# Optimization experiments

Hardware: AMD Instinct MI355X
Metric: run time of the kernel (lower is better)

## Reference

```python
import jax, jax.numpy as jnp
import numpy as np

IN_F, OUT_F, NB = 4096, 4096, 8
BS = IN_F // NB  # 512


def setup_inputs() -> dict:
    key = jax.random.key(0)
    k1, k2, k3, k4 = jax.random.split(key, 4)
    weight = jax.random.normal(k1, (OUT_F, IN_F), dtype=jnp.float32) * 0.02
    bias = jax.random.normal(k2, (OUT_F,), dtype=jnp.float32) * 0.02
    x = jax.random.normal(k3, (4, 2048, IN_F), dtype=jnp.float32)
    R_blocks = jax.random.normal(k4, (NB, BS, BS), dtype=jnp.float32) * 0.1
    return {"weight": weight, "bias": bias, "x": x, "R_blocks": R_blocks, "layer_idx": 0}


def cayley_transform(A):
    # A: [nb, bs, bs]; Q = (I - A_skew) @ inv(I + A_skew + 1e-6 I)
    bs = A.shape[-1]
    I = jnp.eye(bs, dtype=A.dtype)
    A_skew = 0.5 * (A - jnp.swapaxes(A, -2, -1))
    return jnp.matmul(I - A_skew, jnp.linalg.inv(I + A_skew + 1e-6 * I))


def reference(weight, bias, x, R_blocks, layer_idx):
    R_ortho = cayley_transform(R_blocks)  # [nb, bs, bs]
    # weight @ block_diag(R) == per-block contraction on the in_features axis
    w = weight.reshape(OUT_F, NB, BS)
    tw = jnp.einsum('onb,nbc->onc', w, R_ortho).reshape(OUT_F, IN_F)
    # F.linear: x @ tw.T + bias
    out = jnp.einsum('bsi,oi->bso', x, tw) + bias
    return out
```

## Files before the change

### kernel.cpp

```cpp
#include <hip/hip_runtime.h>
#include <hip/hip_bf16.h>


typedef unsigned short u16;
typedef __attribute__((ext_vector_type(8))) __bf16 bf16x8;
typedef __attribute__((ext_vector_type(4))) float f32x4;
typedef __attribute__((ext_vector_type(8))) unsigned short u16x8;
typedef __attribute__((ext_vector_type(4))) unsigned short u16x4;

#define C0   1.000001f
#define C1Q  2.000001f
#define AS1 __attribute__((address_space(1)))
#define AS3 __attribute__((address_space(3)))

__device__ __forceinline__ u16 f2bf(float x) {
  union { float f; unsigned u; } v; v.f = x;
  return (u16)((v.u + 0x7fffu + ((v.u >> 16) & 1u)) >> 16);
}
__device__ __forceinline__ float bf2f(u16 h) {
  union { float f; unsigned u; } v; v.u = ((unsigned)h) << 16; return v.f;
}

__global__ __launch_bounds__(256) void k_build_M(const float* __restrict__ R,
                                                 u16* __restrict__ Mh,
                                                 u16* __restrict__ Ml) {
  __shared__ float t1[32][33];
  const int n = blockIdx.z;
  const int tr = blockIdx.y * 32, tc = blockIdx.x * 32;
  const int ly = threadIdx.x >> 5, lx = threadIdx.x & 31;
  const float* Rb = R + (size_t)n * 262144;
  float a[4];
#pragma unroll
  for (int i = 0; i < 4; ++i) {
    a[i] = Rb[(size_t)(tr + ly + i * 8) * 512 + tc + lx];
    t1[ly + i * 8][lx] = Rb[(size_t)(tc + ly + i * 8) * 512 + tr + lx];
  }
  __syncthreads();
#pragma unroll
  for (int i = 0; i < 4; ++i) {
    const int r = tr + ly + i * 8, c = tc + lx;
    float m = 0.5f * (a[i] - t1[lx][ly + i * 8]) + (r == c ? C0 : 0.0f);
    u16 h = f2bf(m);
    const size_t idx = (size_t)n * 262144 + (size_t)r * 512 + c;
    Mh[idx] = h;
    Ml[idx] = f2bf(m - bf2f(h));
  }
}

__global__ __launch_bounds__(1024) void k_frob_alpha(const u16* __restrict__ G4,
                                                     float* __restrict__ alpha) {
  __shared__ float red[16];
  const int n = blockIdx.x, tid = threadIdx.x;
  const u16* src = G4 + (size_t)n * 262144;
  float s = 0.f;
  for (int i = tid; i < 32768; i += 1024) {
    u16x8 v = reinterpret_cast<const u16x8*>(src)[i];
#pragma unroll
    for (int e = 0; e < 8; ++e) { float f = bf2f(v[e]); s += f * f; }
  }
  for (int off = 32; off; off >>= 1) s += __shfl_down(s, off, 64);
  if ((tid & 63) == 0) red[tid >> 6] = s;
  __syncthreads();
  if (tid == 0) {
    float t = 0.f;
    for (int q = 0; q < 16; ++q) t += red[q];
    float lam = powf(t, 0.125f);
    alpha[n] = 2.0f / (C0 * C0 + lam);
  }
}

__global__ __launch_bounds__(256) void k_init_X0(const u16* __restrict__ Mh,
                                                 const u16* __restrict__ Ml,
                                                 const float* __restrict__ alpha,
                                                 u16* __restrict__ X0,
                                                 u16* __restrict__ X0t) {
  int idx = blockIdx.x * 256 + threadIdx.x;
  int n = idx >> 18, r = (idx >> 9) & 511, c = idx & 511;
  float m = bf2f(Mh[idx]) + bf2f(Ml[idx]);
  float a = alpha[n];
  X0[idx]  = f2bf(a * ((r == c ? 2.0f * C0 : 0.0f) - m));
  X0t[idx] = f2bf(a * m);
}

template <int PROD3, int DMODE, int OMODE>
__global__ __launch_bounds__(256)
void k_bmm(const u16* __restrict__ Ah, const u16* __restrict__ Al,
           const u16* __restrict__ Bh, const u16* __restrict__ Bl,
           const u16* __restrict__ Dh, const u16* __restrict__ Dl,
           u16* __restrict__ Cnh, u16* __restrict__ Cnl,
           u16* __restrict__ Cth, u16* __restrict__ Ctl,
           float* __restrict__ Cf, float cd, float cs) {
  __shared__ __align__(16) u16 sAh[2048], sBh[2048];
  __shared__ __align__(16) u16 sAl[PROD3 ? 2048 : 8], sBl[PROD3 ? 2048 : 8];
  const size_t zb = (size_t)blockIdx.z * 262144;
  const int tid = threadIdx.x, lane = tid & 63, wave = tid >> 6;
  const int m0 = blockIdx.y * 64, n0 = blockIdx.x * 64;
  const int wr = wave >> 1, wc = wave & 1;
  const int c15 = lane & 15, lk = lane >> 4;
  const int srow = tid >> 2;
  const int sg = (tid & 3) ^ (srow & 3);
  f32x4 acc[2][2] = {};
  const u16* pa = Ah + zb + (size_t)(m0 + srow) * 512 + sg * 8;
  const u16* pb = Bh + zb + (size_t)(n0 + srow) * 512 + sg * 8;

  for (int k0 = 0; k0 < 512; k0 += 32) {
    __builtin_amdgcn_global_load_lds((const AS1 void*)(pa + k0),
                                     (AS3 void*)(sAh + (size_t)tid * 8), 16, 0, 0);
    __builtin_amdgcn_global_load_lds((const AS1 void*)(pb + k0),
                                     (AS3 void*)(sBh + (size_t)tid * 8), 16, 0, 0);
    if constexpr (PROD3) {
      const u16* pal = Al + zb + (size_t)(m0 + srow) * 512 + sg * 8;
      const u16* pbl = Bl + zb + (size_t)(n0 + srow) * 512 + sg * 8;
      __builtin_amdgcn_global_load_lds((const AS1 void*)(pal + k0),
                                       (AS3 void*)(sAl + (size_t)tid * 8), 16, 0, 0);
      __builtin_amdgcn_global_load_lds((const AS1 void*)(pbl + k0),
                                       (AS3 void*)(sBl + (size_t)tid * 8), 16, 0, 0);
    }
    __syncthreads();
    bf16x8 a[2], b[2], al2[2], bl2[2];
#pragma unroll
    for (int i = 0; i < 2; ++i) {
      const int fr = wr * 32 + i * 16 + c15;
      const int ia = fr * 32 + ((lk ^ (fr & 3)) * 8);
      a[i] = *reinterpret_cast<const bf16x8*>(&sAh[ia]);
      if constexpr (PROD3) al2[i] = *reinterpret_cast<const bf16x8*>(&sAl[ia]);
    }
#pragma unroll
    for (int j = 0; j < 2; ++j) {
      const int fc = wc * 32 + j * 16 + c15;
      const int ib = fc * 32 + ((lk ^ (fc & 3)) * 8);
      b[j] = *reinterpret_cast<const bf16x8*>(&sBh[ib]);
      if constexpr (PROD3) bl2[j] = *reinterpret_cast<const bf16x8*>(&sBl[ib]);
    }
#pragma unroll
    for (int i = 0; i < 2; ++i)
#pragma unroll
      for (int j = 0; j < 2; ++j) {
        acc[i][j] = __builtin_amdgcn_mfma_f32_16x16x32_bf16(a[i], b[j], acc[i][j], 0, 0, 0);
        if constexpr (PROD3) {
          acc[i][j] = __builtin_amdgcn_mfma_f32_16x16x32_bf16(a[i],   bl2[j], acc[i][j], 0, 0, 0);
          acc[i][j] = __builtin_amdgcn_mfma_f32_16x16x32_bf16(al2[i], b[j],   acc[i][j], 0, 0, 0);
        }
      }
    __syncthreads();
  }
#pragma unroll
  for (int i = 0; i < 2; ++i)
#pragma unroll
    for (int j = 0; j < 2; ++j) {
      const int rowb = m0 + wr * 32 + i * 16 + lk * 4;
      const int col  = n0 + wc * 32 + j * 16 + c15;
      u16 hv[4], lv[4];
#pragma unroll
      for (int r = 0; r < 4; ++r) {
        float val = cs * acc[i][j][r];
        if constexpr (DMODE >= 1) {
          float d = bf2f(Dh[zb + (size_t)(rowb + r) * 512 + col]);
          if constexpr (DMODE == 2) d += bf2f(Dl[zb + (size_t)(rowb + r) * 512 + col]);
          val += cd * d;
        }
        if constexpr (OMODE & 16) Cf[zb + (size_t)(rowb + r) * 512 + col] = val;
        u16 h = f2bf(val);
        if constexpr (OMODE & 1) Cnh[zb + (size_t)(rowb + r) * 512 + col] = h;
        u16 l = 0;
        if constexpr (OMODE & 10) l = f2bf(val - bf2f(h));
        if constexpr (OMODE & 2) Cnl[zb + (size_t)(rowb + r) * 512 + col] = l;
        hv[r] = h; lv[r] = l;
      }
      if constexpr (OMODE & 4) {
        u16x4 v; v[0] = hv[0]; v[1] = hv[1]; v[2] = hv[2]; v[3] = hv[3];
        *reinterpret_cast<u16x4*>(&Cth[zb + (size_t)col * 512 + rowb]) = v;
      }
      if constexpr (OMODE & 8) {
        u16x4 v; v[0] = lv[0]; v[1] = lv[1]; v[2] = lv[2]; v[3] = lv[3];
        *reinterpret_cast<u16x4*>(&Ctl[zb + (size_t)col * 512 + rowb]) = v;
      }
    }
}

template <int SPLIT, int BF16OUT>
__global__ __launch_bounds__(256)
void k_smm(const float* __restrict__ A, int lda, long long astride,
           const float* __restrict__ B, int ldb, long long bstride,
           void* __restrict__ Cv, int ldc, long long cstride,
           const float* __restrict__ D, int ldd, long long dstride,
           float c1, float sgn, int K) {
  __shared__ __align__(16) u16 lA  [128 * 40];
  __shared__ __align__(16) u16 lBT [128 * 40];
  const int nz = blockIdx.z;
  const float* Ab = A + (size_t)nz * astride;
  const float* Bb = B + (size_t)nz * bstride;
  const float* Db = D + (size_t)nz * dstride;
  const int tid = threadIdx.x, lane = tid & 63, wave = tid >> 6;
  const int m0 = blockIdx.y * 128, n0 = blockIdx.x * 128;
  const int wr = wave >> 1, wc = wave & 1;
  f32x4 acc[4][4] = {};

  for (int k0 = 0; k0 < K; k0 += 32) {
    if (k0) __syncthreads();
    {
      const int row = tid >> 1, ks = (tid & 1) * 16;
      const float* src = Ab + (size_t)(m0 + row) * lda + k0 + ks;
      float fv[16];
#pragma unroll
      for (int q = 0; q < 4; ++q) {
        float4 f = *(reinterpret_cast<const float4*>(src) + q);
        fv[q * 4 + 0] = f.x; fv[q * 4 + 1] = f.y; fv[q * 4 + 2] = f.z; fv[q * 4 + 3] = f.w;
      }
      u16x8 w0, w1;
#pragma unroll
      for (int e = 0; e < 8; ++e) { w0[e] = f2bf(fv[e]); w1[e] = f2bf(fv[e + 8]); }
      *reinterpret_cast<u16x8*>(&lA[row * 40 + ks])     = w0;
      *reinterpret_cast<u16x8*>(&lA[row * 40 + ks + 8]) = w1;
    }
    {
      const int kk = tid >> 3, nb = (tid & 7) * 16;
      const float* src = Bb + (size_t)(k0 + kk) * ldb + n0 + nb;
      float fv[16];
#pragma unroll
      for (int q = 0; q < 4; ++q) {
        float4 f = *(reinterpret_cast<const float4*>(src) + q);
        fv[q * 4 + 0] = f.x; fv[q * 4 + 1] = f.y; fv[q * 4 + 2] = f.z; fv[q * 4 + 3] = f.w;
      }
#pragma unroll
      for (int e = 0; e < 16; ++e) lBT[(nb + e) * 40 + kk] = f2bf(fv[e]);
    }
    __syncthreads();
    const int ks = (lane >> 4) * 8;
    bf16x8 af[4], bfr[4];
#pragma unroll
    for (int f = 0; f < 4; ++f) {
      const int ar = wr * 64 + f * 16 + (lane & 15);
      const int bc = wc * 64 + f * 16 + (lane & 15);
      af[f]  = *reinterpret_cast<const bf16x8*>(&lA [ar * 40 + ks]);
      bfr[f] = *reinterpret_cast<const bf16x8*>(&lBT[bc * 40 + ks]);
    }
#pragma unroll
    for (int i = 0; i < 4; ++i)
#pragma unroll
      for (int j = 0; j < 4; ++j)
        acc[i][j] = __builtin_amdgcn_mfma_f32_16x16x32_bf16(af[i], bfr[j], acc[i][j], 0, 0, 0);
  }
#pragma unroll
  for (int i = 0; i < 4; ++i) {
    const int rowb = m0 + wr * 64 + i * 16 + ((lane >> 4) << 2);
#pragma unroll
    for (int j = 0; j < 4; ++j) {
      const int col = n0 + wc * 64 + j * 16 + (lane & 15);
#pragma unroll
      for (int r = 0; r < 4; ++r) {
        float val = sgn * acc[i][j][r];
        if (c1 != 0.0f) val += c1 * Db[(size_t)(rowb + r) * ldd + col];
        if constexpr (BF16OUT)
          reinterpret_cast<u16*>(Cv)[(size_t)nz * cstride + (size_t)(rowb + r) * ldc + col] = f2bf(val);
        else
          reinterpret_cast<float*>(Cv)[(size_t)nz * cstride + (size_t)(rowb + r) * ldc + col] = val;
      }
    }
  }
}

__global__ __launch_bounds__(256) void k_f32_to_bf16(const float* __restrict__ in,
                                                     u16* __restrict__ out) {
  int idx = blockIdx.x * 256 + threadIdx.x;
  const float* src = in + (size_t)idx * 8;
  float4 f0 = *reinterpret_cast<const float4*>(src);
  float4 f1 = *reinterpret_cast<const float4*>(src + 4);
  u16x8 w;
  w[0] = f2bf(f0.x); w[1] = f2bf(f0.y); w[2] = f2bf(f0.z); w[3] = f2bf(f0.w);
  w[4] = f2bf(f1.x); w[5] = f2bf(f1.y); w[6] = f2bf(f1.z); w[7] = f2bf(f1.w);
  *reinterpret_cast<u16x8*>(out + (size_t)idx * 8) = w;
}

#define NSLOT 9

#define RD_B(dst, G)                                                           \
  _Pragma("unroll")                                                            \
  for (int n = 0; n < 4; ++n)                                                  \
    dst[n] = *reinterpret_cast<const bf16x8*>(                                 \
        &lds[bslot * 8192 + (bro + n * 16) * 64 + (G) * 8]);

#define RD_A(dst, MH, G)                                                       \
  _Pragma("unroll")                                                            \
  for (int m = 0; m < 4; ++m)                                                  \
    dst[m] = *reinterpret_cast<const bf16x8*>(                                 \
        &lds[aslot * 8192 + ((MH) * 64 + m * 16 + c15) * 64 + (G) * 8]);

#define MFMA16(afX, bfX, MH)                                                   \
  __builtin_amdgcn_s_setprio(1);                                               \
  _Pragma("unroll")                                                            \
  for (int m = 0; m < 4; ++m)                                                  \
    _Pragma("unroll")                                                          \
    for (int n = 0; n < 4; ++n)                                                \
      acc[(MH) * 4 + m][n] = __builtin_amdgcn_mfma_f32_16x16x32_bf16(          \
          afX[m], bfX[n], acc[(MH) * 4 + m][n], 0, 0, 0);                      \
  __builtin_amdgcn_s_setprio(0);                                               \
  __builtin_amdgcn_sched_barrier(0);

#define SBAR() __builtin_amdgcn_s_barrier();
#define SCHB() __builtin_amdgcn_sched_barrier(0);

#define TILEBODY(WM, LAST)                                                     \
  {                              \
    STAGE();                                                                   \
    RD_A(afB, 1, gsA)                                                          \
    SCHB()                                                                     \
    MFMA16(afA, bf0, 0)                                                        \
    SBAR()                                                                     \
                             \
    STAGE();                                                                   \
    RD_B(bf1, gsB)                                                             \
    RD_A(afA, 0, gsB)                                                          \
    SCHB()                                                                     \
    MFMA16(afB, bf0, 1)                                                        \
    SBAR()                                                                     \
                                 \
    STAGE();                                                                   \
    RD_A(afB, 1, gsB)                                                          \
    SCHB()                                                                     \
    MFMA16(afA, bf1, 0)                                                        \
    SBAR()                                                                     \
        \
    STAGE();                                                                   \
    if ((WM) == 1) { asm volatile("s_waitcnt vmcnt(2)" ::: "memory"); SCHB() } \
    if ((WM) == 2) { asm volatile("s_waitcnt vmcnt(0)" ::: "memory"); SCHB() } \
    SBAR()                                                                     \
    ADV()                                                                      \
    if (!(LAST)) { RD_B(bf0, gsA) RD_A(afA, 0, gsA) }                          \
    SCHB()                                                                     \
    MFMA16(afB, bf1, 1)                                                        \
    SBAR()                                                                     \
  }

#define ADV()                                                                  \
  aslot += 4; if (aslot >= NSLOT) aslot -= NSLOT;                              \
  bslot += 4; if (bslot >= NSLOT) bslot -= NSLOT;

__global__ __launch_bounds__(512, 2)
void k_gemm256(const u16* __restrict__ A, const u16* __restrict__ B,
               const float* __restrict__ bias,
               float* __restrict__ C, int N, int K) {
  __shared__ __align__(16) u16 lds[NSLOT * 8192];
  const int tid = threadIdx.x, lane = tid & 63, wave = tid >> 6;
  int bid = blockIdx.y * gridDim.x + blockIdx.x;
  const int cpx = (gridDim.x * gridDim.y) >> 3;
  bid = (bid & 7) * cpx + (bid >> 3);
  const int nbx = N >> 8;
  const int bx = bid % nbx, by = bid / nbx;
  const int m0 = by << 8, n0 = bx << 8;
  const int wr = wave >> 2, wc = wave & 3;
  const int srow = tid >> 3;
  const int scg  = (tid & 7) ^ (srow & 7);
  const int c15 = lane & 15, lq = lane >> 4;
  const int gs0 = lq ^ (lane & 7);
  const int gsA = gs0, gsB = gs0 ^ 4;
  const int bro = (wc & 1) * 64 + c15;
  const int NT = K >> 6;

  f32x4 acc[8][4] = {};
  bf16x8 afA[4], afB[4], bf0[4], bf1[4];

  int jn = 0, jslot = 0;
  auto STAGE = [&]() {
    if (jn < 4 * NT) {
      const int tau_s = jn >> 2, qh = jn & 3;
      const u16* srcb = (qh < 2)
          ? A + (size_t)(m0 + (qh & 1) * 128 + srow) * (size_t)K
          : B + (size_t)(n0 + (qh & 1) * 128 + srow) * (size_t)K;
      const u16* src = srcb + (tau_s << 6) + scg * 8;
      u16* dst = (u16*)lds + jslot * 8192 + wave * 512;
      __builtin_amdgcn_global_load_lds(
          (const AS1 void*)src, (AS3 void*)dst, 16, 0, 0);
      __builtin_amdgcn_global_load_lds(
          (const AS1 void*)(src + (size_t)64 * K), (AS3 void*)(dst + 4096), 16, 0, 0);
    }
    ++jn; jslot = (jslot == NSLOT - 1) ? 0 : jslot + 1;
  };

  STAGE(); STAGE(); STAGE(); STAGE(); STAGE(); STAGE();
  asm volatile("s_waitcnt vmcnt(4)" ::: "memory");
  SCHB()
  SBAR()
  int aslot = wr, bslot = 2 + (wc >> 1);
  RD_B(bf0, gsA)
  RD_A(afA, 0, gsA)
  SCHB()

  for (int tau = 0; tau < NT - 2; ++tau) {
    TILEBODY(1, 0)
  }
  TILEBODY(2, 0)
  TILEBODY(0, 1)

#pragma unroll
  for (int n = 0; n < 4; ++n) {
    const int col = n0 + wc * 64 + n * 16 + c15;
    const float bv = bias[col];
#pragma unroll
    for (int mi = 0; mi < 8; ++mi) {
      const int rowb = m0 + wr * 128 + mi * 16 + (lq << 2);
#pragma unroll
      for (int r = 0; r < 4; ++r)
        C[(size_t)(rowb + r) * N + col] = acc[mi][n][r] + bv;
    }
  }
}

extern "C" void kernel_launch(void* const* d_in, const int* in_sizes, int n_in,
                              void* d_out, int out_size, void* d_ws, size_t ws_size,
                              hipStream_t stream) {
  const float* W    = (const float*)d_in[0];
  const float* bias = (const float*)d_in[1];
  const float* x    = (const float*)d_in[2];
  const float* R    = (const float*)d_in[3];
  float* out = (float*)d_out;

  char* ws = (char*)d_ws;
  u16* x_bf = (u16*)(ws);
  u16* tw   = (u16*)(ws + 67108864);

  char* arena = (char*)d_out;
  auto slot = [&](int i) -> u16* { return (u16*)(arena + (size_t)i * 4194304); };
  u16 *Mh = slot(0), *Ml = slot(1);
  u16 *G = slot(2), *G2 = slot(3), *G4 = slot(4);
  u16 *Xa = slot(5), *Xat = slot(6), *Xb = slot(7), *Xbt = slot(8);
  u16 *Xbl = slot(9), *Xbtl = slot(10);
  u16 *Tt = slot(2);
  u16 *Tth = slot(3), *Ttl = slot(4);
  u16 *X6h = slot(5), *X6l = slot(6);
  u16 *X6th = slot(11), *X6tl = slot(12);
  float* Qf = (float*)(arena + (size_t)13 * 4194304);
  float* alpha = (float*)(arena + (size_t)15 * 4194304);

  const long long BS2 = 262144;
  const dim3 g8(8, 8, 8);
  const u16* NUL = nullptr;

  k_build_M<<<dim3(16, 16, 8), 256, 0, stream>>>(R, Mh, Ml);
  k_bmm<0, 0, 1><<<g8, 256, 0, stream>>>(Mh, NUL, Mh, NUL, NUL, NUL,
                                         G, nullptr, nullptr, nullptr, nullptr, 0.f, 1.f);
  k_bmm<0, 0, 1><<<g8, 256, 0, stream>>>(G, NUL, G, NUL, NUL, NUL,
                                         G2, nullptr, nullptr, nullptr, nullptr, 0.f, 1.f);
  k_bmm<0, 0, 1><<<g8, 256, 0, stream>>>(G2, NUL, G2, NUL, NUL, NUL,
                                         G4, nullptr, nullptr, nullptr, nullptr, 0.f, 1.f);
  k_frob_alpha<<<8, 1024, 0, stream>>>(G4, alpha);
  k_init_X0<<<8192, 256, 0, stream>>>(Mh, Ml, alpha, Xa, Xat);

  u16 *cur = Xa, *curt = Xat, *nxt = Xb, *nxtt = Xbt;
  for (int it = 0; it < 4; ++it) {
    k_bmm<0, 0, 4><<<g8, 256, 0, stream>>>(Mh, NUL, curt, NUL, NUL, NUL,
                                           nullptr, nullptr, Tt, nullptr, nullptr, 0.f, 1.f);
    k_bmm<0, 1, 5><<<g8, 256, 0, stream>>>(cur, NUL, Tt, NUL, cur, NUL,
                                           nxt, nullptr, nxtt, nullptr, nullptr, 2.f, -1.f);
    u16* t;
    t = cur; cur = nxt; nxt = t;
    t = curt; curt = nxtt; nxtt = t;
  }
  k_bmm<0, 0, 4><<<g8, 256, 0, stream>>>(Mh, NUL, curt, NUL, NUL, NUL,
                                         nullptr, nullptr, Tt, nullptr, nullptr, 0.f, 1.f);
  k_bmm<0, 1, 15><<<g8, 256, 0, stream>>>(cur, NUL, Tt, NUL, cur, NUL,
                                          Xb, Xbl, Xbt, Xbtl, nullptr, 2.f, -1.f);
  k_bmm<1, 0, 12><<<g8, 256, 0, stream>>>(Mh, Ml, Xbt, Xbtl, NUL, NUL,
                                          nullptr, nullptr, Tth, Ttl, nullptr, 0.f, 1.f);
  k_bmm<1, 2, 15><<<g8, 256, 0, stream>>>(Xb, Xbl, Tth, Ttl, Xb, Xbl,
                                          X6h, X6l, X6th, X6tl, nullptr, 2.f, -1.f);
  k_bmm<1, 2, 16><<<g8, 256, 0, stream>>>(Mh, Ml, X6th, X6tl, X6h, X6l,
                                          nullptr, nullptr, nullptr, nullptr, Qf, C1Q, -1.f);
  k_smm<0, 1><<<dim3(4, 32, 8), 256, 0, stream>>>(W, 4096, 512, Qf, 512, BS2,
                                                  tw, 4096, 512, W, 4096, 512, 0.f, 1.f, 512);
  k_f32_to_bf16<<<16384, 256, 0, stream>>>(x, x_bf);
  k_gemm256<<<dim3(16, 32), 512, 0, stream>>>(x_bf, tw, bias, out, 4096, 4096);
}
```

Measured before the change: 583.2 us.

## Switch GEMM main loop to 32-wide K tiles with deeper 18-slot LDS ring

Restructures the bf16 GEMM pipeline so each K step covers 32 elements instead of 64. The LDS ring becomes 18 smaller slots holding several K-tiles of prefetch, each stage issues one async global-to-LDS load per thread, and the swizzle and fragment reads are adjusted to the 32-wide rows. Barriers drop from four per 64-K tile to one per 32-K tile, and the A/B fragment double-buffering is simplified to a single B fragment set. Each wave now issues fewer MFMAs per barrier and does less intra-tile prefetch of fragments, so latency hiding depends more on the deeper global prefetch.

```diff
diff --git a/kernel.cpp b/kernel.cpp
--- a/kernel.cpp
+++ b/kernel.cpp
@@ -272,19 +272,19 @@
   *reinterpret_cast<u16x8*>(out + (size_t)idx * 8) = w;
 }
 
-#define NSLOT 9
-
-#define RD_B(dst, G)                                                           \
+#define NSL 18
+
+#define RD_A3(dst, MH)                                                         \
+  _Pragma("unroll")                                                            \
+  for (int m = 0; m < 4; ++m)                                                  \
+    dst[m] = *reinterpret_cast<const bf16x8*>(                                 \
+        &lds[aslot * 4096 + ((MH) * 64 + m * 16 + c15) * 32 + gsw * 8]);
+
+#define RD_B3(dst)                                                             \
   _Pragma("unroll")                                                            \
   for (int n = 0; n < 4; ++n)                                                  \
     dst[n] = *reinterpret_cast<const bf16x8*>(                                 \
-        &lds[bslot * 8192 + (bro + n * 16) * 64 + (G) * 8]);
-
-#define RD_A(dst, MH, G)                                                       \
-  _Pragma("unroll")                                                            \
-  for (int m = 0; m < 4; ++m)                                                  \
-    dst[m] = *reinterpret_cast<const bf16x8*>(                                 \
-        &lds[aslot * 8192 + ((MH) * 64 + m * 16 + c15) * 64 + (G) * 8]);
+        &lds[bslot * 4096 + (bq64 + n * 16 + c15) * 32 + gsw * 8]);
 
 #define MFMA16(afX, bfX, MH)                                                   \
   __builtin_amdgcn_s_setprio(1);                                               \
@@ -294,53 +294,34 @@
     for (int n = 0; n < 4; ++n)                                                \
       acc[(MH) * 4 + m][n] = __builtin_amdgcn_mfma_f32_16x16x32_bf16(          \
           afX[m], bfX[n], acc[(MH) * 4 + m][n], 0, 0, 0);                      \
-  __builtin_amdgcn_s_setprio(0);                                               \
-  __builtin_amdgcn_sched_barrier(0);
-
-#define SBAR() __builtin_amdgcn_s_barrier();
-#define SCHB() __builtin_amdgcn_sched_barrier(0);
-
-#define TILEBODY(WM, LAST)                                                     \
-  {                              \
-    STAGE();                                                                   \
-    RD_A(afB, 1, gsA)                                                          \
-    SCHB()                                                                     \
-    MFMA16(afA, bf0, 0)                                                        \
-    SBAR()                                                                     \
-                             \
-    STAGE();                                                                   \
-    RD_B(bf1, gsB)                                                             \
-    RD_A(afA, 0, gsB)                                                          \
-    SCHB()                                                                     \
-    MFMA16(afB, bf0, 1)                                                        \
-    SBAR()                                                                     \
-                                 \
-    STAGE();                                                                   \
-    RD_A(afB, 1, gsB)                                                          \
-    SCHB()                                                                     \
-    MFMA16(afA, bf1, 0)                                                        \
-    SBAR()                                                                     \
-        \
-    STAGE();                                                                   \
-    if ((WM) == 1) { asm volatile("s_waitcnt vmcnt(2)" ::: "memory"); SCHB() } \
-    if ((WM) == 2) { asm volatile("s_waitcnt vmcnt(0)" ::: "memory"); SCHB() } \
-    SBAR()                                                                     \
-    ADV()                                                                      \
-    if (!(LAST)) { RD_B(bf0, gsA) RD_A(afA, 0, gsA) }                          \
-    SCHB()                                                                     \
-    MFMA16(afB, bf1, 1)                                                        \
-    SBAR()                                                                     \
-  }
-
-#define ADV()                                                                  \
-  aslot += 4; if (aslot >= NSLOT) aslot -= NSLOT;                              \
-  bslot += 4; if (bslot >= NSLOT) bslot -= NSLOT;
+  __builtin_amdgcn_s_setprio(0);
+
+#define TILE32(WM)                                                             \
+  {                                                                            \
+    int aslot = s0 + wr;            if (aslot >= NSL) aslot -= NSL;            \
+    int bslot = s0 + 2 + (wc >> 1); if (bslot >= NSL) bslot -= NSL;            \
+    STAGE(); STAGE();                                                          \
+    RD_B3(bfr)                                                                 \
+    RD_A3(afA, 0)                                                              \
+    MFMA16(afA, bfr, 0)                                                        \
+    STAGE(); STAGE();                                                          \
+    RD_A3(afB, 1)                                                              \
+    MFMA16(afB, bfr, 1)                                                        \
+    if ((WM) == 1) asm volatile("s_waitcnt vmcnt(8)" ::: "memory");            \
+    if ((WM) == 2) asm volatile("s_waitcnt vmcnt(4)" ::: "memory");            \
+    if ((WM) == 3) asm volatile("s_waitcnt vmcnt(0)" ::: "memory");            \
+    if ((WM) != 0) {                                                           \
+      __builtin_amdgcn_s_barrier();                                            \
+      __builtin_amdgcn_sched_barrier(0);                                       \
+    }                                                                          \
+    s0 += 4; if (s0 >= NSL) s0 -= NSL;                                         \
+  }
 
 __global__ __launch_bounds__(512, 2)
 void k_gemm256(const u16* __restrict__ A, const u16* __restrict__ B,
                const float* __restrict__ bias,
                float* __restrict__ C, int N, int K) {
-  __shared__ __align__(16) u16 lds[NSLOT * 8192];
+  __shared__ __align__(16) u16 lds[NSL * 4096];
   const int tid = threadIdx.x, lane = tid & 63, wave = tid >> 6;
   int bid = blockIdx.y * gridDim.x + blockIdx.x;
   const int cpx = (gridDim.x * gridDim.y) >> 3;
@@ -349,48 +330,44 @@
   const int bx = bid % nbx, by = bid / nbx;
   const int m0 = by << 8, n0 = bx << 8;
   const int wr = wave >> 2, wc = wave & 3;
-  const int srow = tid >> 3;
-  const int scg  = (tid & 7) ^ (srow & 7);
+  const int srow = tid >> 2;
+  const int sgc  = (tid & 3) ^ ((srow >> 1) & 3);
   const int c15 = lane & 15, lq = lane >> 4;
-  const int gs0 = lq ^ (lane & 7);
-  const int gsA = gs0, gsB = gs0 ^ 4;
-  const int bro = (wc & 1) * 64 + c15;
-  const int NT = K >> 6;
+  const int gsw = lq ^ ((c15 >> 1) & 3);
+  const int bq64 = (wc & 1) * 64;
+  const int NT = K >> 5;
 
   f32x4 acc[8][4] = {};
-  bf16x8 afA[4], afB[4], bf0[4], bf1[4];
-
-  int jn = 0, jslot = 0;
+  bf16x8 afA[4], afB[4], bfr[4];
+
+  int jn = 0, js = 0;
   auto STAGE = [&]() {
     if (jn < 4 * NT) {
-      const int tau_s = jn >> 2, qh = jn & 3;
-      const u16* srcb = (qh < 2)
-          ? A + (size_t)(m0 + (qh & 1) * 128 + srow) * (size_t)K
-          : B + (size_t)(n0 + (qh & 1) * 128 + srow) * (size_t)K;
-      const u16* src = srcb + (tau_s << 6) + scg * 8;
-      u16* dst = (u16*)lds + jslot * 8192 + wave * 512;
+      const int t = jn >> 2, q = jn & 3;
+      const u16* srcb = (q < 2)
+          ? A + (size_t)(m0 + q * 128 + srow) * (size_t)K
+          : B + (size_t)(n0 + (q - 2) * 128 + srow) * (size_t)K;
+      const u16* src = srcb + (t << 5) + sgc * 8;
+      u16* dst = (u16*)lds + js * 4096 + tid * 8;
       __builtin_amdgcn_global_load_lds(
           (const AS1 void*)src, (AS3 void*)dst, 16, 0, 0);
-      __builtin_amdgcn_global_load_lds(
-          (const AS1 void*)(src + (size_t)64 * K), (AS3 void*)(dst + 4096), 16, 0, 0);
-    }
-    ++jn; jslot = (jslot == NSLOT - 1) ? 0 : jslot + 1;
+    }
+    ++jn; js = (js == NSL - 1) ? 0 : js + 1;
   };
 
-  STAGE(); STAGE(); STAGE(); STAGE(); STAGE(); STAGE();
-  asm volatile("s_waitcnt vmcnt(4)" ::: "memory");
-  SCHB()
-  SBAR()
-  int aslot = wr, bslot = 2 + (wc >> 1);
-  RD_B(bf0, gsA)
-  RD_A(afA, 0, gsA)
-  SCHB()
-
-  for (int tau = 0; tau < NT - 2; ++tau) {
-    TILEBODY(1, 0)
-  }
-  TILEBODY(2, 0)
-  TILEBODY(0, 1)
+#pragma unroll
+  for (int i = 0; i < 12; ++i) STAGE();
+  asm volatile("s_waitcnt vmcnt(8)" ::: "memory");
+  __builtin_amdgcn_s_barrier();
+  __builtin_amdgcn_sched_barrier(0);
+
+  int s0 = 0;
+  for (int tau = 0; tau < NT - 3; ++tau) {
+    TILE32(1)
+  }
+  TILE32(2)
+  TILE32(3)
+  TILE32(0)
 
 #pragma unroll
   for (int n = 0; n < 4; ++n) {
```

Result: no change. 574.8 us (-1.4%).
